# Kernel optimization log

Measured on AMD Instinct MI355X. Metric: run time of the kernel, lower is better.

Reference implementation:

```python
import jax, jax.numpy as jnp
import numpy as np

IMG = 512
STRIDE = 16
K = 9
FM = IMG // STRIDE          # 32
N = FM * FM * K             # 9216 anchors
IOU_THR = 0.7
POST_NMS_TOPK = 300
C_FEAT = 512


def _conv(x, w, b, stride=1, padding='SAME'):
    y = jax.lax.conv_general_dilated(x, w, (stride, stride), padding,
                                     dimension_numbers=('NCHW', 'OIHW', 'NCHW'))
    return y + b[None, :, None, None]


def _make_anchors():
    scales = [64.0, 128.0, 256.0]
    ratios = [0.5, 1.0, 2.0]
    wh = np.array([[s * np.sqrt(r), s / np.sqrt(r)] for s in scales for r in ratios],
                  np.float32)                                    # [K,2]
    ctr = (np.arange(FM, dtype=np.float32) + 0.5) * STRIDE
    cy, cx = np.meshgrid(ctr, ctr, indexing='ij')               # [FM,FM]
    c = np.stack([cx, cy], -1)[:, :, None, :]                   # [FM,FM,1,2]
    half = wh[None, None, :, :] / 2.0                           # [1,1,K,2]
    boxes = np.concatenate([c - half, c + half], -1)            # [FM,FM,K,4]
    return boxes.reshape(-1, 4)


def setup_inputs():
    key = jax.random.key(0)
    ks = jax.random.split(key, 5)
    p = lambda k, shp, s: jax.random.normal(k, shp, jnp.float32) * s
    return {
        'input_image': jax.random.normal(ks[0], (1, 3, IMG, IMG), jnp.float32),
        'anchors': jnp.asarray(_make_anchors()),
        'w_bb': p(ks[1], (C_FEAT, 3, STRIDE, STRIDE), 0.05),
        'b_bb': jnp.zeros((C_FEAT,), jnp.float32),
        'w_rpn': p(ks[2], (C_FEAT, C_FEAT, 3, 3), 0.02),
        'b_rpn': jnp.zeros((C_FEAT,), jnp.float32),
        'w_cls': p(ks[3], (2 * K, C_FEAT, 1, 1), 0.01),
        'b_cls': jnp.zeros((2 * K,), jnp.float32),
        'w_box': p(ks[4], (4 * K, C_FEAT, 1, 1), 0.01),
        'b_box': jnp.zeros((4 * K,), jnp.float32),
    }


def _decode_clip(anchors, deltas):
    # apply_delta_to_anchors + clip_boxes
    wa = anchors[:, 2] - anchors[:, 0]
    ha = anchors[:, 3] - anchors[:, 1]
    cxa = anchors[:, 0] + 0.5 * wa
    cya = anchors[:, 1] + 0.5 * ha
    dx, dy = deltas[:, 0], deltas[:, 1]
    dw = jnp.clip(deltas[:, 2], -4.0, 4.0)   # numeric guard on exp
    dh = jnp.clip(deltas[:, 3], -4.0, 4.0)
    cx = cxa + dx * wa
    cy = cya + dy * ha
    w = wa * jnp.exp(dw)
    h = ha * jnp.exp(dh)
    x1 = jnp.maximum(cx - 0.5 * w, 0.0)
    y1 = jnp.maximum(cy - 0.5 * h, 0.0)
    x2 = jnp.minimum(cx + 0.5 * w, IMG - 1.0)
    y2 = jnp.minimum(cy + 0.5 * h, IMG - 1.0)
    return jnp.stack([x1, y1, x2, y2], -1)


def _iou_matrix(b):
    x1, y1, x2, y2 = b[:, 0], b[:, 1], b[:, 2], b[:, 3]
    area = (x2 - x1) * (y2 - y1)
    iw = jnp.clip(jnp.minimum(x2[:, None], x2[None, :]) - jnp.maximum(x1[:, None], x1[None, :]), 0.0)
    ih = jnp.clip(jnp.minimum(y2[:, None], y2[None, :]) - jnp.maximum(y1[:, None], y1[None, :]), 0.0)
    inter = iw * ih
    return inter / (area[:, None] + area[None, :] - inter + 1e-9)


def _nms_keep(boxes_sorted):
    # boxes_sorted: [N,4] in descending score order; greedy hard NMS.
    iou = jax.lax.stop_gradient(_iou_matrix(boxes_sorted))  # [N,N]
    idx = jnp.arange(N)

    def body(i, keep):
        sup = keep[i] & (iou[i] > IOU_THR) & (idx > i)
        return keep & ~sup

    return jax.lax.fori_loop(0, N, body, jnp.ones((N,), bool))


def reference(input_image, anchors, w_bb, b_bb, w_rpn, b_rpn, w_cls, b_cls, w_box, b_box):
    # backbone
    feat = jax.nn.relu(_conv(input_image, w_bb, b_bb, stride=STRIDE, padding='VALID'))  # [1,512,32,32]
    # rpn
    hid = jax.nn.relu(_conv(feat, w_rpn, b_rpn))
    cls = _conv(hid, w_cls, b_cls)   # [1,2K,FM,FM]
    box = _conv(hid, w_box, b_box)   # [1,4K,FM,FM]
    # foreground scores: cls_scores[:, k:, :, :]
    scores = cls[0, K:, :, :].transpose(1, 2, 0).reshape(-1)                    # [N]
    deltas = box[0].reshape(K, 4, FM, FM).transpose(2, 3, 0, 1).reshape(-1, 4)  # [N,4]
    proposals = _decode_clip(anchors, deltas)
    order = jnp.argsort(-scores)
    boxes_s = proposals[order]
    keep = _nms_keep(boxes_s)
    # first 300 kept boxes (score order); fixed shape via stable argsort on keep flag
    sel = jnp.argsort((~keep).astype(jnp.int32), stable=True)[:POST_NMS_TOPK]
    return boxes_s[sel]
```

## Files before the change

### kernel.cpp

```cpp
#include <hip/hip_runtime.h>
#include <stdint.h>

typedef unsigned long long u64;

#define PTOT 1024
#define CF   512
#define NBOX 9216
#define NW   144
#define TOPK 300

__device__ __forceinline__ uint32_t score_key(float s) {
  uint32_t b = __float_as_uint(s);
  uint32_t o = (b & 0x80000000u) ? ~b : (b | 0x80000000u);
  return ~o;
}

#define FMA16() do { \
  acc[0][0] = fmaf(bv.x, av.x, acc[0][0]); \
  acc[0][1] = fmaf(bv.x, av.y, acc[0][1]); \
  acc[0][2] = fmaf(bv.x, av.z, acc[0][2]); \
  acc[0][3] = fmaf(bv.x, av.w, acc[0][3]); \
  acc[1][0] = fmaf(bv.y, av.x, acc[1][0]); \
  acc[1][1] = fmaf(bv.y, av.y, acc[1][1]); \
  acc[1][2] = fmaf(bv.y, av.z, acc[1][2]); \
  acc[1][3] = fmaf(bv.y, av.w, acc[1][3]); \
  acc[2][0] = fmaf(bv.z, av.x, acc[2][0]); \
  acc[2][1] = fmaf(bv.z, av.y, acc[2][1]); \
  acc[2][2] = fmaf(bv.z, av.z, acc[2][2]); \
  acc[2][3] = fmaf(bv.z, av.w, acc[2][3]); \
  acc[3][0] = fmaf(bv.w, av.x, acc[3][0]); \
  acc[3][1] = fmaf(bv.w, av.y, acc[3][1]); \
  acc[3][2] = fmaf(bv.w, av.z, acc[3][2]); \
  acc[3][3] = fmaf(bv.w, av.w, acc[3][3]); \
} while (0)

__global__ __launch_bounds__(256) void k_wt(const float* __restrict__ w_rpn,
                                            const float* __restrict__ w_bb,
                                            float* __restrict__ wT,
                                            float* __restrict__ wT1) {
  __shared__ float T[32][33];
  int bx = blockIdx.x;
  const float* src; float* dst; int K, kb;
  if (bx < 144) { src = w_rpn; dst = wT; K = 4608; kb = bx * 32; }
  else          { src = w_bb;  dst = wT1; K = 768; kb = (bx - 144) * 32; }
  const int cob = blockIdx.y * 32;
  const int tx = threadIdx.x & 31, ty = threadIdx.x >> 5;
#pragma unroll
  for (int r = 0; r < 32; r += 8)
    T[ty + r][tx] = src[(cob + ty + r) * K + kb + tx];
  __syncthreads();
#pragma unroll
  for (int r = 0; r < 32; r += 8)
    dst[(kb + ty + r) * 512 + cob + tx] = T[tx][ty + r];
}

__global__ __launch_bounds__(256) void k_conv1(const float* __restrict__ img,
                                               const float* __restrict__ wT1,
                                               float* __restrict__ featP) {
  __shared__ __align__(16) float As[32][72];
  __shared__ __align__(16) float Bs[32][64];
  const int t = threadIdx.x;
  const int pbase = blockIdx.x * 64;
  const int cobase = blockIdx.y * 64;
  const int z = blockIdx.z;
  const int pg = t & 15, cg = t >> 4;
  const int pp0 = pg * 4, cc0 = cg * 4;
  const int py0 = pbase >> 5;
  float acc[4][4] = {};
  for (int kb = 0; kb < 256; kb += 32) {
    const int ky0 = kb >> 4;
#pragma unroll
    for (int l0 = 0; l0 < 2048; l0 += 256) {
      int l = l0 + t;
      int seg = l >> 9, off = l & 511;
      int py_off = seg >> 1, ky_off = seg & 1;
      int row = (py0 + py_off) * 16 + ky0 + ky_off;
      float v = img[(z * 512 + row) * 512 + off];
      As[ky_off * 16 + (off & 15)][py_off * 32 + (off >> 4)] = v;
    }
#pragma unroll
    for (int it = 0; it < 2; ++it) {
      int idx4 = it * 256 + t;
      int k = idx4 >> 4, co4 = (idx4 & 15) << 2;
      *(float4*)&Bs[k][co4] =
          *(const float4*)&wT1[(z * 256 + kb + k) * 512 + cobase + co4];
    }
    __syncthreads();
#pragma unroll
    for (int kk = 0; kk < 32; ++kk) {
      float4 av = *(const float4*)&As[kk][pp0];
      float4 bv = *(const float4*)&Bs[kk][cc0];
      FMA16();
    }
    __syncthreads();
  }
#pragma unroll
  for (int i = 0; i < 4; ++i) {
    float* o = &featP[((size_t)z * CF + cobase + cc0 + i) * PTOT + pbase + pp0];
    *(float4*)o = make_float4(acc[i][0], acc[i][1], acc[i][2], acc[i][3]);
  }
}

__global__ __launch_bounds__(256) void k_reduce1(const float* __restrict__ featP,
                                                 const float* __restrict__ bias,
                                                 float* __restrict__ feat) {
  int idx4 = blockIdx.x * 256 + threadIdx.x;
  int co = idx4 >> 8;
  const float4* f = (const float4*)featP;
  float4 a = f[idx4];
  float4 b = f[idx4 + 131072];
  float4 c = f[idx4 + 262144];
  float bb = bias[co];
  float4 o;
  o.x = fmaxf(a.x + b.x + c.x + bb, 0.f);
  o.y = fmaxf(a.y + b.y + c.y + bb, 0.f);
  o.z = fmaxf(a.z + b.z + c.z + bb, 0.f);
  o.w = fmaxf(a.w + b.w + c.w + bb, 0.f);
  ((float4*)feat)[idx4] = o;
}

__global__ __launch_bounds__(256) void k_conv2(const float* __restrict__ feat,
                                               const float* __restrict__ wT,
                                               float* __restrict__ hidP,
                                               int ciPerZ) {
  __shared__ __align__(16) float As[8][6][44];
  __shared__ __align__(16) float Bs[72 * 64];
  const int t = threadIdx.x;
  const int pyb = blockIdx.x * 4;
  const int cob = blockIdx.y * 64;
  const int z = blockIdx.z;
  const int cib = z * ciPerZ;
  const int pg = t & 15, cg = t >> 4;
  const int prow = pg >> 2, px0 = (pg & 3) * 8;
  const int co0 = cg * 4;
  float acc[4][8] = {};
  for (int cc = 0; cc < ciPerZ; cc += 8) {
    {
      int idx4 = t;
#pragma unroll
      for (int it = 0; it < 2; ++it, idx4 += 256) {
        if (idx4 < 480) {
          int ci = idx4 / 60;
          int rem = idx4 - ci * 60;
          int row = rem / 10;
          int col4 = (rem - row * 10) << 2;
          int x = col4 - 4;
          int gy = pyb + row - 1;
          float4 v = make_float4(0.f, 0.f, 0.f, 0.f);
          if (x >= 0 && x < 32 && gy >= 0 && gy < 32)
            v = *(const float4*)&feat[(cib + cc + ci) * PTOT + gy * 32 + x];
          *(float4*)&As[ci][row][col4] = v;
        }
      }
    }
    {
      const int kg0 = (cib + cc) * 9;
      int idx4 = t;
#pragma unroll
      for (int it = 0; it < 5; ++it, idx4 += 256) {
        if (idx4 < 1152) {
          int k = idx4 >> 4;
          int co4 = (idx4 & 15) << 2;
          *(float4*)&Bs[k * 64 + co4] =
              *(const float4*)&wT[(kg0 + k) * 512 + cob + co4];
        }
      }
    }
    __syncthreads();
#pragma unroll 1
    for (int ci = 0; ci < 8; ++ci) {
#pragma unroll
      for (int dy = 0; dy < 3; ++dy) {
        const float* Ar = &As[ci][prow + dy][px0];
        float rw[16];
        *(float4*)&rw[0]  = *(const float4*)&Ar[0];
        *(float4*)&rw[4]  = *(const float4*)&Ar[4];
        *(float4*)&rw[8]  = *(const float4*)&Ar[8];
        *(float4*)&rw[12] = *(const float4*)&Ar[12];
#pragma unroll
        for (int dx = 0; dx < 3; ++dx) {
          const float* Bp = &Bs[(ci * 9 + dy * 3 + dx) * 64 + co0];
          float4 b0 = *(const float4*)&Bp[0];
          float bm[4] = {b0.x, b0.y, b0.z, b0.w};
#pragma unroll
          for (int m = 0; m < 4; ++m)
#pragma unroll
            for (int j = 0; j < 8; ++j)
              acc[m][j] = fmaf(rw[3 + dx + j], bm[m], acc[m][j]);
        }
      }
    }
    __syncthreads();
  }
  const int prowg = pyb + prow;
#pragma unroll
  for (int m = 0; m < 4; ++m) {
    int co = cob + co0 + m;
    float* o = &hidP[((size_t)z * CF + co) * PTOT + prowg * 32 + px0];
    *(float4*)&o[0] = make_float4(acc[m][0], acc[m][1], acc[m][2], acc[m][3]);
    *(float4*)&o[4] = make_float4(acc[m][4], acc[m][5], acc[m][6], acc[m][7]);
  }
}

__global__ __launch_bounds__(256) void k_reduce2(const float* __restrict__ hidP,
                                                 const float* __restrict__ bias,
                                                 float* __restrict__ hid_t, int Z) {
  __shared__ float T[64][65];
  const int co0 = blockIdx.x * 64, p0 = blockIdx.y * 64;
  const int t = threadIdx.x;
#pragma unroll
  for (int it = 0; it < 4; ++it) {
    int idx4 = it * 256 + t;
    int co = idx4 >> 4, p4 = (idx4 & 15) << 2;
    float4 s = make_float4(0.f, 0.f, 0.f, 0.f);
    for (int zz = 0; zz < Z; ++zz) {
      float4 v = *(const float4*)&hidP[((size_t)zz * CF + co0 + co) * PTOT + p0 + p4];
      s.x += v.x; s.y += v.y; s.z += v.z; s.w += v.w;
    }
    float b = bias[co0 + co];
    T[co][p4 + 0] = fmaxf(s.x + b, 0.f);
    T[co][p4 + 1] = fmaxf(s.y + b, 0.f);
    T[co][p4 + 2] = fmaxf(s.z + b, 0.f);
    T[co][p4 + 3] = fmaxf(s.w + b, 0.f);
  }
  __syncthreads();
#pragma unroll
  for (int it = 0; it < 4; ++it) {
    int idx4 = it * 256 + t;
    int p = idx4 >> 4, co4 = (idx4 & 15) << 2;
    float4 o = make_float4(T[co4][p], T[co4 + 1][p], T[co4 + 2][p], T[co4 + 3][p]);
    *(float4*)&hid_t[(size_t)(p0 + p) * CF + co0 + co4] = o;
  }
}

__global__ __launch_bounds__(256) void k_heads(const float* __restrict__ hid_t,
                                               const float* __restrict__ wcls,
                                               const float* __restrict__ bcls,
                                               const float* __restrict__ wbox,
                                               const float* __restrict__ bbox,
                                               float* __restrict__ scores,
                                               float* __restrict__ deltas) {
  const int t = threadIdx.x;
  const int lane = t & 63, w = t >> 6;
  const int p = blockIdx.x * 4 + w;
  const float* hp = &hid_t[(size_t)p * CF + lane * 8];
  float4 h0 = *(const float4*)hp;
  float4 h1 = *(const float4*)(hp + 4);
#pragma unroll 1
  for (int ch = 0; ch < 45; ++ch) {
    const float* wp = (ch < 9) ? &wcls[(9 + ch) * CF] : &wbox[(ch - 9) * CF];
    float4 w0 = *(const float4*)(wp + lane * 8);
    float4 w1 = *(const float4*)(wp + lane * 8 + 4);
    float s = h0.x * w0.x + h0.y * w0.y + h0.z * w0.z + h0.w * w0.w +
              h1.x * w1.x + h1.y * w1.y + h1.z * w1.z + h1.w * w1.w;
#pragma unroll
    for (int off = 32; off >= 1; off >>= 1) s += __shfl_xor(s, off, 64);
    if (lane == 0) {
      if (ch < 9) scores[p * 9 + ch] = s + bcls[9 + ch];
      else        deltas[p * 36 + (ch - 9)] = s + bbox[ch - 9];
    }
  }
}

__global__ __launch_bounds__(256) void k_decode(const float* __restrict__ deltas,
                                                const float* __restrict__ anchors,
                                                float4* __restrict__ props) {
  int n = blockIdx.x * 256 + threadIdx.x;
  float4 a = ((const float4*)anchors)[n];
  float4 d = ((const float4*)deltas)[n];
  float wa = a.z - a.x, ha = a.w - a.y;
  float cxa = a.x + 0.5f * wa, cya = a.y + 0.5f * ha;
  float dw = fminf(fmaxf(d.z, -4.f), 4.f);
  float dh = fminf(fmaxf(d.w, -4.f), 4.f);
  float cx = cxa + d.x * wa, cy = cya + d.y * ha;
  float ww = wa * expf(dw), hh = ha * expf(dh);
  float x1 = fmaxf(cx - 0.5f * ww, 0.f);
  float y1 = fmaxf(cy - 0.5f * hh, 0.f);
  float x2 = fminf(cx + 0.5f * ww, 511.f);
  float y2 = fminf(cy + 0.5f * hh, 511.f);
  props[n] = make_float4(x1, y1, x2, y2);
}

__global__ __launch_bounds__(1024) void k_sort1(const float* __restrict__ scores,
                                                u64* __restrict__ keys) {
  __shared__ u64 lds[8192];
  const int t = threadIdx.x;
  const int base = blockIdx.x * 8192;
  const bool desc = (blockIdx.x == 1);
#pragma unroll
  for (int l0 = 0; l0 < 8192; l0 += 1024) {
    int l = l0 + t, g = base + l;
    u64 kv = ~0ull;
    if (g < NBOX) kv = ((u64)score_key(scores[g]) << 32) | (u64)g;
    lds[l] = kv;
  }
  for (int k = 2; k <= 8192; k <<= 1) {
    for (int j = k >> 1; j > 0; j >>= 1) {
      __syncthreads();
#pragma unroll
      for (int m = 0; m < 4; ++m) {
        int pr = m * 1024 + t;
        int i = ((pr & ~(j - 1)) << 1) | (pr & (j - 1));
        int l2 = i | j;
        bool ascBlk = ((i & k) == 0);
        bool dirAsc = desc ? !ascBlk : ascBlk;
        u64 x = lds[i], y = lds[l2];
        bool sw = dirAsc ? (x > y) : (x < y);
        if (sw) { lds[i] = y; lds[l2] = x; }
      }
    }
  }
  __syncthreads();
#pragma unroll
  for (int l0 = 0; l0 < 8192; l0 += 1024) {
    int l = l0 + t;
    keys[base + l] = lds[l];
  }
}

__global__ __launch_bounds__(256) void k_sort2(u64* __restrict__ keys) {
  int i = blockIdx.x * 256 + threadIdx.x;
  u64 x = keys[i], y = keys[i + 8192];
  if (x > y) { keys[i] = y; keys[i + 8192] = x; }
}

__global__ __launch_bounds__(1024) void k_sort3(const u64* __restrict__ keys,
                                                const float4* __restrict__ props,
                                                float4* __restrict__ boxesS) {
  __shared__ u64 lds[8192];
  const int t = threadIdx.x;
  const int base = blockIdx.x * 8192;
#pragma unroll
  for (int l0 = 0; l0 < 8192; l0 += 1024) {
    int l = l0 + t;
    lds[l] = keys[base + l];
  }
  for (int j = 4096; j > 0; j >>= 1) {
    __syncthreads();
#pragma unroll
    for (int m = 0; m < 4; ++m) {
      int pr = m * 1024 + t;
      int i = ((pr & ~(j - 1)) << 1) | (pr & (j - 1));
      int l2 = i | j;
      u64 x = lds[i], y = lds[l2];
      if (x > y) { lds[i] = y; lds[l2] = x; }
    }
  }
  __syncthreads();
#pragma unroll
  for (int l0 = 0; l0 < 8192; l0 += 1024) {
    int l = l0 + t, g = base + l;
    if (g < NBOX) {
      int idx = (int)(lds[l] & 0xffffffffull);
      boxesS[g] = props[idx];
    }
  }
}

__global__ __launch_bounds__(256) void k_iou(const float4* __restrict__ boxesS,
                                             u64* __restrict__ mask) {
  __shared__ float4 cb[4][64];
  __shared__ float ca[4][64];
  const int t = threadIdx.x;
  const int lane = t & 63, w = t >> 6;
  const int u = blockIdx.x;
  const int v = blockIdx.y * 4 + w + 1;
  int y = u + v; if (y >= 145) y -= 145;
  const int a_ = min(u, y), b_ = max(u, y);
  const int iw = a_, wj = b_ - 1;

  {
    float4 c = boxesS[wj * 64 + lane];
    cb[w][lane] = c;
    ca[w][lane] = (c.z - c.x) * (c.w - c.y);
  }
  __syncthreads();

  const int i = iw * 64 + lane;
  float4 a = boxesS[i];
  float areaA = (a.z - a.x) * (a.w - a.y);
  u64 bits = 0;
#pragma unroll 4
  for (int jj = 0; jj < 64; ++jj) {
    int j = wj * 64 + jj;
    float4 c = cb[w][jj];
    float iw_ = fmaxf(fminf(a.z, c.z) - fmaxf(a.x, c.x), 0.f);
    float ih_ = fmaxf(fminf(a.w, c.w) - fmaxf(a.y, c.y), 0.f);
    float inter = iw_ * ih_;
    float uni = areaA + ca[w][jj] - inter + 1e-9f;
    float thr = 0.7f * uni;
    bool pos = uni > 0.f;
    bool sup = pos && (inter > thr);
    if (pos && (fabsf(inter - thr) <= thr * 1e-5f))
      sup = (inter / uni) > 0.7f;
    bits |= ((u64)(sup && (j > i))) << jj;
  }
  mask[(size_t)i * NW + wj] = bits;
}

__global__ __launch_bounds__(64) void k_scan(const u64* __restrict__ mask,
                                             const float4* __restrict__ boxesS,
                                             float* __restrict__ out) {
  __shared__ u64 Dbuf[64];
  __shared__ u64 keepArr[NW];
  __shared__ int pf[NW + 2];
  __shared__ int outIdx[TOPK];
  const int lane = threadIdx.x;

  u64 r0 = 0, r1 = 0, r2 = 0;
  int keptCount = 0;
  int stopSpan = NW - 1;

  u64 dcur = mask[(size_t)lane * NW];

  for (int wb = 0; wb < NW; ++wb) {
    Dbuf[lane] = dcur;
    __syncthreads();

    u64 v = (wb < 64) ? r0 : ((wb < 128) ? r1 : r2);
    u64 R = __shfl(v, wb & 63, 64);

    u64 dnext = 0;
    if (wb + 1 < NW)
      dnext = mask[(size_t)((wb + 1) * 64 + lane) * NW + (wb + 1)];

    u64 keepmask = 0;
    if (R != ~0ull) {
#pragma unroll
      for (int c = 0; c < 2; ++c) {
        u64 d[32];
#pragma unroll
        for (int r = 0; r < 32; ++r) d[r] = Dbuf[c * 32 + r];
#pragma unroll
        for (int r = 0; r < 32; ++r) {
          int rl = c * 32 + r;
          u64 keep = ((R >> rl) & 1ull) ^ 1ull;
          keepmask |= keep << rl;
          R |= d[r] & (0ull - keep);
        }
      }
      u64 km = keepmask;
      while (km) {
        int first = wb * 64 + __ffsll((long long)km) - 1;
        int idx[8];
#pragma unroll
        for (int s = 0; s < 8; ++s) {
          if (km) { idx[s] = wb * 64 + __ffsll((long long)km) - 1; km &= km - 1; }
          else    { idx[s] = first; }
        }
        u64 A[8], B[8], C[8];
#pragma unroll
        for (int s = 0; s < 8; ++s) {
          const u64* q = mask + (size_t)idx[s] * NW;
          A[s] = q[lane];
          B[s] = q[lane + 64];
          C[s] = (lane < 16) ? q[lane + 128] : 0ull;
        }
#pragma unroll
        for (int s = 0; s < 8; ++s) { r0 |= A[s]; r1 |= B[s]; r2 |= C[s]; }
      }
      keptCount += __popcll(keepmask);
    }
    if (lane == 0) keepArr[wb] = keepmask;
    dcur = dnext;
    if (keptCount >= TOPK) { stopSpan = wb; break; }
  }

  __syncthreads();
  if (lane == 0) {
    int acc = 0;
    for (int s = 0; s <= stopSpan; ++s) { pf[s] = acc; acc += __popcll(keepArr[s]); }
    pf[stopSpan + 1] = acc;
  }
  __syncthreads();
  const int keptTotal = pf[stopSpan + 1];

  for (int s = lane; s <= stopSpan; s += 64) {
    u64 km = keepArr[s];
    int slot = pf[s];
    while (km && slot < TOPK) {
      int rl = __ffsll((long long)km) - 1; km &= km - 1;
      outIdx[slot++] = s * 64 + rl;
    }
  }
  if (keptTotal < TOPK) {
    for (int s = lane; s <= stopSpan; s += 64) {
      u64 rm = ~keepArr[s];
      int slot = keptTotal + s * 64 - pf[s];
      while (rm && slot < TOPK) {
        int rl = __ffsll((long long)rm) - 1; rm &= rm - 1;
        outIdx[slot++] = s * 64 + rl;
      }
    }
  }
  __syncthreads();
#pragma unroll
  for (int k0 = 0; k0 < TOPK + 63; k0 += 64) {
    int k = k0 + lane;
    if (k < TOPK) {
      float4 bx = boxesS[outIdx[k]];
      out[k * 4 + 0] = bx.x;
      out[k * 4 + 1] = bx.y;
      out[k * 4 + 2] = bx.z;
      out[k * 4 + 3] = bx.w;
    }
  }
}

extern "C" void kernel_launch(void* const* d_in, const int* in_sizes, int n_in,
                              void* d_out, int out_size, void* d_ws, size_t ws_size,
                              hipStream_t stream) {
  const float* img   = (const float*)d_in[0];
  const float* anch  = (const float*)d_in[1];
  const float* w_bb  = (const float*)d_in[2];
  const float* b_bb  = (const float*)d_in[3];
  const float* w_rpn = (const float*)d_in[4];
  const float* b_rpn = (const float*)d_in[5];
  const float* w_cls = (const float*)d_in[6];
  const float* b_cls = (const float*)d_in[7];
  const float* w_box = (const float*)d_in[8];
  const float* b_box = (const float*)d_in[9];

  char* ws = (char*)d_ws;
  int Z = 16;
  if (ws_size < 22806528ull + 16ull * 2097152ull) Z = 8;
  if (ws_size < 22806528ull + 8ull * 2097152ull)  Z = 4;
  if (ws_size < 22806528ull + 4ull * 2097152ull)  Z = 2;
  if (ws_size < 22806528ull + 2ull * 2097152ull)  Z = 1;

  float* wT    = (float*)(ws);
  float* wT1   = (float*)(ws + 9437184);
  float* featP = (float*)(ws + 11010048);
  float* feat  = (float*)(ws + 17301504);
  float* hidP  = (float*)(ws + 19398656);
  char*  hte   = ws + 19398656 + (size_t)Z * 2097152;
  float* hid_t = (float*)hte;
  char*  tail  = hte + 2097152;
  float*  scores = (float*)(tail);
  float*  deltas = (float*)(tail + 0x40000);
  float4* props  = (float4*)(tail + 0x80000);
  u64*    keys   = (u64*)(tail + 0xC0000);
  float4* boxesS = (float4*)(tail + 0x100000);
  u64*    mask   = (u64*)(ws + 11010048);
  float*  out    = (float*)d_out;

  hipLaunchKernelGGL(k_wt, dim3(168, 16), dim3(256), 0, stream, w_rpn, w_bb, wT, wT1);
  hipLaunchKernelGGL(k_conv1, dim3(16, 8, 3), dim3(256), 0, stream, img, wT1, featP);
  hipLaunchKernelGGL(k_reduce1, dim3(512), dim3(256), 0, stream, featP, b_bb, feat);
  hipLaunchKernelGGL(k_conv2, dim3(8, 8, Z), dim3(256), 0, stream, feat, wT, hidP, 512 / Z);
  hipLaunchKernelGGL(k_reduce2, dim3(8, 16), dim3(256), 0, stream, hidP, b_rpn, hid_t, Z);
  hipLaunchKernelGGL(k_heads, dim3(256), dim3(256), 0, stream, hid_t, w_cls, b_cls, w_box, b_box, scores, deltas);
  hipLaunchKernelGGL(k_decode, dim3(36), dim3(256), 0, stream, deltas, anch, props);
  hipLaunchKernelGGL(k_sort1, dim3(2), dim3(1024), 0, stream, scores, keys);
  hipLaunchKernelGGL(k_sort2, dim3(32), dim3(256), 0, stream, keys);
  hipLaunchKernelGGL(k_sort3, dim3(2), dim3(1024), 0, stream, keys, props, boxesS);
  hipLaunchKernelGGL(k_iou, dim3(145, 18), dim3(256), 0, stream, boxesS, mask);
  hipLaunchKernelGGL(k_scan, dim3(1), dim3(64), 0, stream, mask, boxesS, out);
}
```

Before: 376.2 us.

## Replace bitonic sort with parallel rank-counting and fused decode scatter

Drops the three-kernel bitonic sort, which ran on only two 1024-thread workgroups and needed many barrier-separated passes. In its place, the heads kernel writes 32-bit order keys directly. A new kernel counts each box's rank by comparing it against every other key, spread over a 37x19 grid, with ties broken by index. A final kernel sums the partial counts, decodes the proposal and writes it straight to its sorted slot, which removes the separate decode pass and the props buffer. This trades O(N log^2 N) barrier-bound work for O(N^2) comparisons that spread across the whole GPU.

After: 306.8 us. 1.23x faster.

```diff
diff --git a/kernel.cpp b/kernel.cpp
--- a/kernel.cpp
+++ b/kernel.cpp
@@ -6,8 +6,10 @@
 #define PTOT 1024
 #define CF   512
 #define NBOX 9216
+#define NPAD 9280
 #define NW   144
 #define TOPK 300
+#define RCH  19
 
 __device__ __forceinline__ uint32_t score_key(float s) {
   uint32_t b = __float_as_uint(s);
@@ -238,9 +240,13 @@
                                                const float* __restrict__ bcls,
                                                const float* __restrict__ wbox,
                                                const float* __restrict__ bbox,
-                                               float* __restrict__ scores,
+                                               uint32_t* __restrict__ key32,
                                                float* __restrict__ deltas) {
   const int t = threadIdx.x;
+  if (blockIdx.x == 256) {
+    if (t < 64) key32[NBOX + t] = 0xFFFFFFFFu;
+    return;
+  }
   const int lane = t & 63, w = t >> 6;
   const int p = blockIdx.x * 4 + w;
   const float* hp = &hid_t[(size_t)p * CF + lane * 8];
@@ -256,18 +262,49 @@
 #pragma unroll
     for (int off = 32; off >= 1; off >>= 1) s += __shfl_xor(s, off, 64);
     if (lane == 0) {
-      if (ch < 9) scores[p * 9 + ch] = s + bcls[9 + ch];
+      if (ch < 9) key32[p * 9 + ch] = score_key(s + bcls[9 + ch]);
       else        deltas[p * 36 + (ch - 9)] = s + bbox[ch - 9];
     }
   }
 }
 
-__global__ __launch_bounds__(256) void k_decode(const float* __restrict__ deltas,
-                                                const float* __restrict__ anchors,
-                                                float4* __restrict__ props) {
-  int n = blockIdx.x * 256 + threadIdx.x;
-  float4 a = ((const float4*)anchors)[n];
-  float4 d = ((const float4*)deltas)[n];
+__global__ __launch_bounds__(256) void k_rank(const uint32_t* __restrict__ key32,
+                                              uint32_t* __restrict__ P) {
+  const int t = threadIdx.x;
+  const int lane = t & 63, w = t >> 6;
+  const int a = blockIdx.x * 4 + w;
+  if (a >= 145) return;
+  const int by = blockIdx.y;
+  const int ig = a * 64 + lane;
+  const uint32_t ka = key32[ig];
+  uint32_t cnt = 0;
+#pragma unroll 1
+  for (int w2 = 0; w2 < 8; ++w2) {
+    int word = by * 8 + w2;
+    if (word >= 145) break;
+    const uint32_t* bk = &key32[word * 64];
+    const int jbase = word * 64;
+#pragma unroll
+    for (int s = 0; s < 64; ++s) {
+      uint32_t kb = bk[s];
+      int j = jbase + s;
+      cnt += (uint32_t)((kb < ka) || (kb == ka && j < ig));
+    }
+  }
+  P[(size_t)by * NPAD + ig] = cnt;
+}
+
+__global__ __launch_bounds__(256) void k_rfin(const uint32_t* __restrict__ P,
+                                              const float* __restrict__ anchors,
+                                              const float* __restrict__ deltas,
+                                              float4* __restrict__ boxesS) {
+  int i = blockIdx.x * 256 + threadIdx.x;
+  if (i >= NBOX) return;
+  uint32_t rank = 0;
+#pragma unroll
+  for (int c = 0; c < RCH; ++c) rank += P[(size_t)c * NPAD + i];
+  float4 a = ((const float4*)anchors)[i];
+  float4 d = ((const float4*)deltas)[i];
   float wa = a.z - a.x, ha = a.w - a.y;
   float cxa = a.x + 0.5f * wa, cya = a.y + 0.5f * ha;
   float dw = fminf(fmaxf(d.z, -4.f), 4.f);
@@ -278,83 +315,7 @@
   float y1 = fmaxf(cy - 0.5f * hh, 0.f);
   float x2 = fminf(cx + 0.5f * ww, 511.f);
   float y2 = fminf(cy + 0.5f * hh, 511.f);
-  props[n] = make_float4(x1, y1, x2, y2);
-}
-
-__global__ __launch_bounds__(1024) void k_sort1(const float* __restrict__ scores,
-                                                u64* __restrict__ keys) {
-  __shared__ u64 lds[8192];
-  const int t = threadIdx.x;
-  const int base = blockIdx.x * 8192;
-  const bool desc = (blockIdx.x == 1);
-#pragma unroll
-  for (int l0 = 0; l0 < 8192; l0 += 1024) {
-    int l = l0 + t, g = base + l;
-    u64 kv = ~0ull;
-    if (g < NBOX) kv = ((u64)score_key(scores[g]) << 32) | (u64)g;
-    lds[l] = kv;
-  }
-  for (int k = 2; k <= 8192; k <<= 1) {
-    for (int j = k >> 1; j > 0; j >>= 1) {
-      __syncthreads();
-#pragma unroll
-      for (int m = 0; m < 4; ++m) {
-        int pr = m * 1024 + t;
-        int i = ((pr & ~(j - 1)) << 1) | (pr & (j - 1));
-        int l2 = i | j;
-        bool ascBlk = ((i & k) == 0);
-        bool dirAsc = desc ? !ascBlk : ascBlk;
-        u64 x = lds[i], y = lds[l2];
-        bool sw = dirAsc ? (x > y) : (x < y);
-        if (sw) { lds[i] = y; lds[l2] = x; }
-      }
-    }
-  }
-  __syncthreads();
-#pragma unroll
-  for (int l0 = 0; l0 < 8192; l0 += 1024) {
-    int l = l0 + t;
-    keys[base + l] = lds[l];
-  }
-}
-
-__global__ __launch_bounds__(256) void k_sort2(u64* __restrict__ keys) {
-  int i = blockIdx.x * 256 + threadIdx.x;
-  u64 x = keys[i], y = keys[i + 8192];
-  if (x > y) { keys[i] = y; keys[i + 8192] = x; }
-}
-
-__global__ __launch_bounds__(1024) void k_sort3(const u64* __restrict__ keys,
-                                                const float4* __restrict__ props,
-                                                float4* __restrict__ boxesS) {
-  __shared__ u64 lds[8192];
-  const int t = threadIdx.x;
-  const int base = blockIdx.x * 8192;
-#pragma unroll
-  for (int l0 = 0; l0 < 8192; l0 += 1024) {
-    int l = l0 + t;
-    lds[l] = keys[base + l];
-  }
-  for (int j = 4096; j > 0; j >>= 1) {
-    __syncthreads();
-#pragma unroll
-    for (int m = 0; m < 4; ++m) {
-      int pr = m * 1024 + t;
-      int i = ((pr & ~(j - 1)) << 1) | (pr & (j - 1));
-      int l2 = i | j;
-      u64 x = lds[i], y = lds[l2];
-      if (x > y) { lds[i] = y; lds[l2] = x; }
-    }
-  }
-  __syncthreads();
-#pragma unroll
-  for (int l0 = 0; l0 < 8192; l0 += 1024) {
-    int l = l0 + t, g = base + l;
-    if (g < NBOX) {
-      int idx = (int)(lds[l] & 0xffffffffull);
-      boxesS[g] = props[idx];
-    }
-  }
+  boxesS[rank] = make_float4(x1, y1, x2, y2);
 }
 
 __global__ __launch_bounds__(256) void k_iou(const float4* __restrict__ boxesS,
@@ -536,24 +497,21 @@
   char*  hte   = ws + 19398656 + (size_t)Z * 2097152;
   float* hid_t = (float*)hte;
   char*  tail  = hte + 2097152;
-  float*  scores = (float*)(tail);
-  float*  deltas = (float*)(tail + 0x40000);
-  float4* props  = (float4*)(tail + 0x80000);
-  u64*    keys   = (u64*)(tail + 0xC0000);
-  float4* boxesS = (float4*)(tail + 0x100000);
-  u64*    mask   = (u64*)(ws + 11010048);
-  float*  out    = (float*)d_out;
+  float*    deltas = (float*)(tail);
+  uint32_t* key32  = (uint32_t*)(tail + 0x28000);
+  float4*   boxesS = (float4*)(tail + 0x38000);
+  uint32_t* P      = (uint32_t*)(ws + 11010048);
+  u64*      mask   = (u64*)(ws + 11010048);
+  float*    out    = (float*)d_out;
 
   hipLaunchKernelGGL(k_wt, dim3(168, 16), dim3(256), 0, stream, w_rpn, w_bb, wT, wT1);
   hipLaunchKernelGGL(k_conv1, dim3(16, 8, 3), dim3(256), 0, stream, img, wT1, featP);
   hipLaunchKernelGGL(k_reduce1, dim3(512), dim3(256), 0, stream, featP, b_bb, feat);
   hipLaunchKernelGGL(k_conv2, dim3(8, 8, Z), dim3(256), 0, stream, feat, wT, hidP, 512 / Z);
   hipLaunchKernelGGL(k_reduce2, dim3(8, 16), dim3(256), 0, stream, hidP, b_rpn, hid_t, Z);
-  hipLaunchKernelGGL(k_heads, dim3(256), dim3(256), 0, stream, hid_t, w_cls, b_cls, w_box, b_box, scores, deltas);
-  hipLaunchKernelGGL(k_decode, dim3(36), dim3(256), 0, stream, deltas, anch, props);
-  hipLaunchKernelGGL(k_sort1, dim3(2), dim3(1024), 0, stream, scores, keys);
-  hipLaunchKernelGGL(k_sort2, dim3(32), dim3(256), 0, stream, keys);
-  hipLaunchKernelGGL(k_sort3, dim3(2), dim3(1024), 0, stream, keys, props, boxesS);
+  hipLaunchKernelGGL(k_heads, dim3(257), dim3(256), 0, stream, hid_t, w_cls, b_cls, w_box, b_box, key32, deltas);
+  hipLaunchKernelGGL(k_rank, dim3(37, RCH), dim3(256), 0, stream, key32, P);
+  hipLaunchKernelGGL(k_rfin, dim3(37), dim3(256), 0, stream, P, anch, deltas, boxesS);
   hipLaunchKernelGGL(k_iou, dim3(145, 18), dim3(256), 0, stream, boxesS, mask);
   hipLaunchKernelGGL(k_scan, dim3(1), dim3(64), 0, stream, mask, boxesS, out);
 }
```
